# Optimization experiments

Hardware: AMD Instinct MI355X
Metric: run time of the kernel (lower is better)

## Reference

```python
import jax, jax.numpy as jnp
import numpy as np
import math

H, N, B, L = 512, 32, 4, 2048


def setup_inputs() -> dict:
    key = jax.random.key(0)
    ks = jax.random.split(key, 6)
    log_dt_min, log_dt_max = math.log(0.001), math.log(0.01)
    log_dt = jax.random.uniform(ks[0], (H,)) * (log_dt_max - log_dt_min) + log_dt_min
    # A = -0.5 + i*pi*n  =>  log_A_real = log(0.5), A_imag = pi*n
    log_A_real = jnp.full((H, N), math.log(0.5), dtype=jnp.float32)
    A_imag = jnp.broadcast_to(math.pi * jnp.arange(N, dtype=jnp.float32), (H, N))
    # B = ones (complex) stored as real/imag pair
    B_ri = jnp.stack([jnp.ones((N,)), jnp.zeros((N,))], axis=-1).astype(jnp.float32)
    C_ri = jax.random.normal(ks[1], (H, N, 2), dtype=jnp.float32)
    D = jax.random.normal(ks[2], (H,), dtype=jnp.float32)
    W1 = jax.random.normal(ks[3], (H, H), dtype=jnp.float32)
    W2 = jax.random.normal(ks[4], (H, H), dtype=jnp.float32)
    x = jax.random.normal(ks[5], (B, L, H), dtype=jnp.float32)
    return {"input": x, "log_dt": log_dt, "log_A_real": log_A_real,
            "A_imag": A_imag, "B_ri": B_ri, "C_ri": C_ri, "D": D,
            "W1": W1, "W2": W2}


def reference(input, log_dt, log_A_real, A_imag, B_ri, C_ri, D, W1, W2):
    dt = jnp.exp(log_dt)                             # (H,)
    A = -jnp.exp(log_A_real) + 1j * A_imag           # (H,N) complex64
    dtA = (0.5 * dt)[:, None] * A                    # (H,N)
    Ad = (1.0 + dtA) / (1.0 - dtA)                   # bilinear (GBT alpha=0.5) discrete A
    Bc = B_ri[:, 0] + 1j * B_ri[:, 1]                # (N,)
    Bd = dt[:, None] * Bc[None, :] / (1.0 - dtA)     # (H,N) discrete B
    C = C_ri[..., 0] + 1j * C_ri[..., 1]             # (H,N)

    us = jnp.swapaxes(input, 0, 1)                   # (L,B,H)
    x0 = jnp.zeros(input.shape[0:1] + Ad.shape, dtype=Ad.dtype)  # (B,H,N)

    def step(x, u):
        # x: (B,H,N) complex state; u: (B,H) input at one timestep
        x = Ad[None] * x + Bd[None] * u[:, :, None]
        y = jnp.einsum('hn,bhn->bh', C, x).real + D * u
        return x, y

    _, ys = jax.lax.scan(step, x0, us)               # ys: (L,B,H)
    y = jnp.swapaxes(ys, 0, 1)                       # (B,L,H)
    # GLU over stacked projections: (y@W1) * sigmoid(y@W2)
    return (y @ W1) * jax.nn.sigmoid(y @ W2)
```

## Files before the change

### kernel.cpp

```cpp
#include <hip/hip_runtime.h>

#define H_ 512
#define N_ 32
#define B_ 4
#define L_ 2048
#define LC 128
#define NC 16

typedef _Float16 f16x8 __attribute__((ext_vector_type(8)));
typedef float f32x4 __attribute__((ext_vector_type(4)));

__device__ inline unsigned short f2h(float f) {
  _Float16 h = (_Float16)f;
  return __builtin_bit_cast(unsigned short, h);
}
__device__ inline float2 cmul(float2 a, float2 b) {
  return make_float2(fmaf(a.x, b.x, -(a.y * b.y)), fmaf(a.x, b.y, a.y * b.x));
}

#define GLD_LDS16(gsrc, ldst)                                                        \
  __builtin_amdgcn_global_load_lds(                                                  \
      (const __attribute__((address_space(1))) unsigned int*)(gsrc),                 \
      (__attribute__((address_space(3))) unsigned int*)(ldst), 16, 0, 0)

__global__ void transpose_k(const float* __restrict__ in, unsigned short* __restrict__ out) {
  __shared__ float tile[32][33];
  int b = blockIdx.z;
  int t0 = blockIdx.x * 32;
  int h0 = blockIdx.y * 32;
  int tx = threadIdx.x, ty = threadIdx.y;
  const float* src = in + (size_t)b * L_ * H_;
#pragma unroll
  for (int i = 0; i < 32; i += 8)
    tile[ty + i][tx] = src[(size_t)(t0 + ty + i) * H_ + h0 + tx];
  __syncthreads();
  unsigned short* dst = out + (size_t)b * H_ * L_;
#pragma unroll
  for (int i = 0; i < 32; i += 8)
    dst[(size_t)(h0 + ty + i) * L_ + t0 + tx] = f2h(tile[tx][ty + i]);
}

__global__ void wtrans_k(const float* __restrict__ W1, const float* __restrict__ W2,
                         unsigned short* __restrict__ WT1, unsigned short* __restrict__ WT2) {
  __shared__ float tile[32][33];
  const float* W = blockIdx.z ? W2 : W1;
  unsigned short* WT = blockIdx.z ? WT2 : WT1;
  int k0 = blockIdx.x * 32, j0 = blockIdx.y * 32;
  int tx = threadIdx.x, ty = threadIdx.y;
#pragma unroll
  for (int i = 0; i < 32; i += 8)
    tile[ty + i][tx] = W[(size_t)(k0 + ty + i) * H_ + j0 + tx];
  __syncthreads();
#pragma unroll
  for (int i = 0; i < 32; i += 8)
    WT[(size_t)(j0 + ty + i) * H_ + k0 + tx] = f2h(tile[tx][ty + i]);
}

__global__ void ytrans_k(const unsigned short* __restrict__ in, unsigned short* __restrict__ out) {
  __shared__ unsigned short tile[32][34];
  int b = blockIdx.z;
  int t0 = blockIdx.x * 32;
  int h0 = blockIdx.y * 32;
  int tx = threadIdx.x, ty = threadIdx.y;
  const unsigned short* src = in + (size_t)b * H_ * L_;
#pragma unroll
  for (int i = 0; i < 32; i += 8)
    tile[ty + i][tx] = src[(size_t)(h0 + ty + i) * L_ + t0 + tx];
  __syncthreads();
  unsigned short* dst = out + (size_t)b * L_ * H_;
#pragma unroll
  for (int i = 0; i < 32; i += 8)
    dst[(size_t)(t0 + ty + i) * H_ + h0 + tx] = tile[tx][ty + i];
}

#define O_U   0
#define O_BIG 17408
#define O_XEND (O_BIG + 17408)
#define O_XS  52224
#define O_KV  61440
__global__ __launch_bounds__(256) void toeplitz_k(
    const unsigned short* __restrict__ xT,
    const float* __restrict__ log_dt,
    const float* __restrict__ log_A_real,
    const float* __restrict__ A_imag,
    const float* __restrict__ B_ri,
    const float* __restrict__ C_ri,
    const float* __restrict__ Dv,
    unsigned short* __restrict__ yT) {
  __shared__ __align__(16) char slds[61952];
  int h = blockIdx.x;
  int tid = threadIdx.x;
  int wave = tid >> 6, lane = tid & 63;
  int wm = wave >> 1, wn = wave & 1;

  int n = tid & 31, s = tid >> 5;
  float dtv = expf(log_dt[h]);
  float2 Ad, Bd, Cc;
  {
    int idx = (h << 5) + n;
    float ar = -expf(log_A_real[idx]);
    float ai = A_imag[idx];
    float dr = 0.5f * dtv * ar, di = 0.5f * dtv * ai;
    float omr = 1.0f - dr;
    float inv = 1.0f / (omr * omr + di * di);
    Ad = make_float2((1.0f - dr * dr - di * di) * inv, 2.0f * di * inv);
    float br = B_ri[2 * n], bi = B_ri[2 * n + 1];
    Bd = make_float2(dtv * (br * omr - bi * di) * inv, dtv * (br * di + bi * omr) * inv);
    float2 c = ((const float2*)C_ri)[idx];
    Cc = make_float2(c.x, c.y);
  }
  float2 Ad16 = Ad;
#pragma unroll
  for (int q = 0; q < 4; ++q) Ad16 = cmul(Ad16, Ad16);
  float2 AdS = make_float2(1.f, 0.f);
  for (int q = 0; q < s; ++q) AdS = cmul(AdS, Ad16);

  {
    float2 cur = cmul(AdS, Bd);
#pragma unroll
    for (int jj = 0; jj < 16; ++jj) {
      int col = 127 - (s * 16 + jj);
      *(unsigned short*)(slds + O_BIG + n * 272 + col * 2) = f2h(cur.x);
      *(unsigned short*)(slds + O_BIG + (32 + n) * 272 + col * 2) = f2h(cur.y);
      cur = cmul(cur, Ad);
    }
  }
  {
    int bc = tid >> 2, q = tid & 3;
    const uint4* src = (const uint4*)(xT + ((size_t)(bc >> 4) * H_ + h) * L_ + (bc & 15) * 128);
#pragma unroll
    for (int i = 0; i < 4; ++i) {
      uint4 v = src[q * 4 + i];
      *(uint4*)(slds + O_U + bc * 272 + (q * 4 + i) * 16) = v;
    }
  }
  __syncthreads();

  {
    f32x4 acc0[2][2];
#pragma unroll
    for (int mf = 0; mf < 2; ++mf)
#pragma unroll
      for (int nf = 0; nf < 2; ++nf) { f32x4 z; z[0]=z[1]=z[2]=z[3]=0.f; acc0[mf][nf]=z; }
#pragma unroll
    for (int ks = 0; ks < 4; ++ks) {
      int kb = ks * 64 + (lane >> 4) * 16;
      f16x8 a[2], bfr[2];
#pragma unroll
      for (int mf = 0; mf < 2; ++mf)
        a[mf] = *(const f16x8*)(slds + O_BIG + (wm * 32 + mf * 16 + (lane & 15)) * 272 + kb);
#pragma unroll
      for (int nf = 0; nf < 2; ++nf)
        bfr[nf] = *(const f16x8*)(slds + O_U + (wn * 32 + nf * 16 + (lane & 15)) * 272 + kb);
#pragma unroll
      for (int mf = 0; mf < 2; ++mf)
#pragma unroll
        for (int nf = 0; nf < 2; ++nf)
          acc0[mf][nf] = __builtin_amdgcn_mfma_f32_16x16x32_f16(a[mf], bfr[nf], acc0[mf][nf], 0, 0, 0);
    }
    __syncthreads();
#pragma unroll
    for (int mf = 0; mf < 2; ++mf)
#pragma unroll
      for (int nf = 0; nf < 2; ++nf)
#pragma unroll
        for (int r = 0; r < 4; ++r) {
          int row = wm * 32 + mf * 16 + (lane >> 4) * 4 + r;
          int col = wn * 32 + nf * 16 + (lane & 15);
          *(float*)(slds + O_XEND + (row * 68 + col) * 4) = acc0[mf][nf][r];
        }
  }
  __syncthreads();

  if (tid < 128) {
    int nn = tid & 31, b = tid >> 5;
    float2 Ap = Ad;
#pragma unroll
    for (int q = 0; q < 7; ++q) Ap = cmul(Ap, Ap);
    float2 X = make_float2(0.f, 0.f);
    for (int c = 0; c < NC; ++c) {
      int bc = b * 16 + c;
      unsigned int w = (unsigned int)f2h(X.x) | ((unsigned int)f2h(X.y) << 16);
      *(unsigned int*)(slds + O_XS + bc * 144 + nn * 4) = w;
      float er = *(const float*)(slds + O_XEND + (nn * 68 + bc) * 4);
      float ei = *(const float*)(slds + O_XEND + ((32 + nn) * 68 + bc) * 4);
      X = make_float2(fmaf(Ap.x, X.x, fmaf(-Ap.y, X.y, er)),
                      fmaf(Ap.x, X.y, fmaf(Ap.y, X.x, ei)));
    }
  }
  __syncthreads();

  {
    float2 cur = cmul(cmul(Cc, Bd), AdS);
#pragma unroll
    for (int jj = 0; jj < 16; ++jj) {
      int tau = s * 16 + jj;
      *(float*)(slds + O_BIG + (tau * 33 + n) * 4) = cur.x;
      cur = cmul(cur, Ad);
    }
  }
  __syncthreads();
  if (tid < 128) {
    float acc = 0.f;
#pragma unroll
    for (int q = 0; q < 32; ++q)
      acc += *(const float*)(slds + O_BIG + (tid * 33 + q) * 4);
    *(float*)(slds + O_KV + tid * 4) = acc;
  }
  __syncthreads();

  {
    float Dh = Dv[h];
    const float* kv = (const float*)(slds + O_KV);
    int t = tid >> 1, j0 = (tid & 1) * 64;
#pragma unroll
    for (int g = 0; g < 16; ++g) {
      int j = j0 + g * 4;
      unsigned short e[4];
#pragma unroll
      for (int ee = 0; ee < 4; ++ee) {
        int jj = j + ee;
        float v = 0.f;
        if (jj <= t) v = (jj == t) ? (kv[0] + Dh) : kv[t - jj];
        e[ee] = f2h(v);
      }
      unsigned int w0 = (unsigned int)e[0] | ((unsigned int)e[1] << 16);
      unsigned int w1 = (unsigned int)e[2] | ((unsigned int)e[3] << 16);
      *(uint2*)(slds + O_BIG + t * 272 + j * 2) = make_uint2(w0, w1);
    }
  }
  __syncthreads();

  f32x4 accy[4][2];
#pragma unroll
  for (int mf = 0; mf < 4; ++mf)
#pragma unroll
    for (int nf = 0; nf < 2; ++nf) { f32x4 z; z[0]=z[1]=z[2]=z[3]=0.f; accy[mf][nf]=z; }
#pragma unroll
  for (int ks = 0; ks < 4; ++ks) {
    int kb = ks * 64 + (lane >> 4) * 16;
    f16x8 a[4], bfr[2];
#pragma unroll
    for (int mf = 0; mf < 4; ++mf)
      a[mf] = *(const f16x8*)(slds + O_BIG + (wm * 64 + mf * 16 + (lane & 15)) * 272 + kb);
#pragma unroll
    for (int nf = 0; nf < 2; ++nf)
      bfr[nf] = *(const f16x8*)(slds + O_U + (wn * 32 + nf * 16 + (lane & 15)) * 272 + kb);
#pragma unroll
    for (int mf = 0; mf < 4; ++mf)
#pragma unroll
      for (int nf = 0; nf < 2; ++nf)
        accy[mf][nf] = __builtin_amdgcn_mfma_f32_16x16x32_f16(a[mf], bfr[nf], accy[mf][nf], 0, 0, 0);
  }
  __syncthreads();

  {
    float2 cur = cmul(cmul(Cc, Ad), AdS);
#pragma unroll
    for (int jj = 0; jj < 16; ++jj) {
      int t = s * 16 + jj;
      unsigned int w = (unsigned int)f2h(cur.x) | ((unsigned int)f2h(-cur.y) << 16);
      *(unsigned int*)(slds + O_BIG + t * 144 + n * 4) = w;
      cur = cmul(cur, Ad);
    }
  }
  __syncthreads();

#pragma unroll
  for (int ks = 0; ks < 2; ++ks) {
    int kb = ks * 64 + (lane >> 4) * 16;
    f16x8 a[4], bfr[2];
#pragma unroll
    for (int mf = 0; mf < 4; ++mf)
      a[mf] = *(const f16x8*)(slds + O_BIG + (wm * 64 + mf * 16 + (lane & 15)) * 144 + kb);
#pragma unroll
    for (int nf = 0; nf < 2; ++nf)
      bfr[nf] = *(const f16x8*)(slds + O_XS + (wn * 32 + nf * 16 + (lane & 15)) * 144 + kb);
#pragma unroll
    for (int mf = 0; mf < 4; ++mf)
#pragma unroll
      for (int nf = 0; nf < 2; ++nf)
        accy[mf][nf] = __builtin_amdgcn_mfma_f32_16x16x32_f16(a[mf], bfr[nf], accy[mf][nf], 0, 0, 0);
  }
  __syncthreads();

#pragma unroll
  for (int mf = 0; mf < 4; ++mf)
#pragma unroll
    for (int nf = 0; nf < 2; ++nf)
#pragma unroll
      for (int r = 0; r < 4; ++r) {
        int t = wm * 64 + mf * 16 + (lane >> 4) * 4 + r;
        int bc = wn * 32 + nf * 16 + (lane & 15);
        *(float*)(slds + O_BIG + (t * 68 + bc) * 4) = accy[mf][nf][r];
      }
  __syncthreads();
  {
    int bc = tid >> 2, tl = tid & 3;
    unsigned short* dst = yT + ((size_t)(bc >> 4) * H_ + h) * L_ + (bc & 15) * 128;
#pragma unroll
    for (int tt = 0; tt < 16; ++tt) {
      int t = tl * 32 + tt * 2;
      float v0 = *(const float*)(slds + O_BIG + (t * 68 + bc) * 4);
      float v1 = *(const float*)(slds + O_BIG + ((t + 1) * 68 + bc) * 4);
      unsigned int w = (unsigned int)f2h(v0) | ((unsigned int)f2h(v1) << 16);
      *(unsigned int*)(dst + t) = w;
    }
  }
}

__global__ __launch_bounds__(256) void glu_gemm_k(const unsigned short* __restrict__ yN,
                                                  const unsigned short* __restrict__ WT1,
                                                  const unsigned short* __restrict__ WT2,
                                                  float* __restrict__ out) {
  __shared__ __align__(16) char lds[24576];
  int tid = threadIdx.x;
  int m0 = blockIdx.x * 64;
  int n0 = blockIdx.y * 64;
  int wave = tid >> 6, lane = tid & 63;
  int wm = wave >> 1, wn = wave & 1;
  int srow = tid >> 3;
  int scb = (tid & 7) * 16;

  f32x4 acc1[2][2], acc2[2][2];
#pragma unroll
  for (int mf = 0; mf < 2; ++mf)
#pragma unroll
    for (int nf = 0; nf < 2; ++nf) {
      f32x4 z; z[0]=z[1]=z[2]=z[3]=0.f;
      acc1[mf][nf] = z; acc2[mf][nf] = z;
    }

  const char* ybase = (const char*)yN;
  const char* b1base = (const char*)WT1;
  const char* b2base = (const char*)WT2;
  char* As_ = lds;
  char* B1_ = lds + 8192;
  char* B2_ = lds + 16384;

  for (int k0 = 0; k0 < H_; k0 += 64) {
#pragma unroll
    for (int i = 0; i < 2; ++i) {
      int row = i * 32 + srow;
      int sc = scb ^ ((row & 7) << 4);
      GLD_LDS16(ybase + ((size_t)(m0 + row) * H_ + k0) * 2 + sc, As_ + wave * 1024 + i * 4096);
      GLD_LDS16(b1base + ((size_t)(n0 + row) * H_ + k0) * 2 + sc, B1_ + wave * 1024 + i * 4096);
      GLD_LDS16(b2base + ((size_t)(n0 + row) * H_ + k0) * 2 + sc, B2_ + wave * 1024 + i * 4096);
    }
    __syncthreads();
#pragma unroll
    for (int ks = 0; ks < 2; ++ks) {
      f16x8 a[2], b1[2], b2[2];
      int kb = ks * 64 + (lane >> 4) * 16;
#pragma unroll
      for (int mf = 0; mf < 2; ++mf) {
        int row = wm * 32 + mf * 16 + (lane & 15);
        a[mf] = *(const f16x8*)(As_ + row * 128 + (kb ^ ((row & 7) << 4)));
      }
#pragma unroll
      for (int nf = 0; nf < 2; ++nf) {
        int row = wn * 32 + nf * 16 + (lane & 15);
        int off = row * 128 + (kb ^ ((row & 7) << 4));
        b1[nf] = *(const f16x8*)(B1_ + off);
        b2[nf] = *(const f16x8*)(B2_ + off);
      }
#pragma unroll
      for (int mf = 0; mf < 2; ++mf)
#pragma unroll
        for (int nf = 0; nf < 2; ++nf) {
          acc1[mf][nf] = __builtin_amdgcn_mfma_f32_16x16x32_f16(a[mf], b1[nf], acc1[mf][nf], 0, 0, 0);
          acc2[mf][nf] = __builtin_amdgcn_mfma_f32_16x16x32_f16(a[mf], b2[nf], acc2[mf][nf], 0, 0, 0);
        }
    }
    __syncthreads();
  }
  int nb = n0 + wn * 32 + (lane & 15);
  int rbase = (lane >> 4) * 4;
#pragma unroll
  for (int mf = 0; mf < 2; ++mf)
#pragma unroll
    for (int nf = 0; nf < 2; ++nf)
#pragma unroll
      for (int r = 0; r < 4; ++r) {
        int m = m0 + wm * 32 + mf * 16 + rbase + r;
        float g1 = acc1[mf][nf][r];
        float g2 = acc2[mf][nf][r];
        out[(size_t)m * H_ + nb + nf * 16] = g1 / (1.0f + __expf(-g2));
      }
}

extern "C" void kernel_launch(void* const* d_in, const int* in_sizes, int n_in,
                              void* d_out, int out_size, void* d_ws, size_t ws_size,
                              hipStream_t stream) {
  (void)in_sizes; (void)n_in; (void)out_size; (void)ws_size;
  const float* x          = (const float*)d_in[0];
  const float* log_dt     = (const float*)d_in[1];
  const float* log_A_real = (const float*)d_in[2];
  const float* A_imag     = (const float*)d_in[3];
  const float* B_ri       = (const float*)d_in[4];
  const float* C_ri       = (const float*)d_in[5];
  const float* Dv         = (const float*)d_in[6];
  const float* W1         = (const float*)d_in[7];
  const float* W2         = (const float*)d_in[8];
  float* out = (float*)d_out;
  char* ws = (char*)d_ws;

  unsigned short* yN   = (unsigned short*)(ws);
  unsigned short* xT16 = (unsigned short*)(ws + (8u << 20));
  unsigned short* yT   = (unsigned short*)(ws + (16u << 20));
  unsigned short* WT1  = (unsigned short*)(ws + (24u << 20));
  unsigned short* WT2  = (unsigned short*)(ws + (24u << 20) + (512u << 10));

  dim3 tblock(32, 8);
  transpose_k<<<dim3(L_ / 32, H_ / 32, B_), tblock, 0, stream>>>(x, xT16);
  wtrans_k<<<dim3(16, 16, 2), tblock, 0, stream>>>(W1, W2, WT1, WT2);

  toeplitz_k<<<H_, 256, 0, stream>>>(xT16, log_dt, log_A_real, A_imag, B_ri, C_ri, Dv, yT);

  ytrans_k<<<dim3(L_ / 32, H_ / 32, B_), tblock, 0, stream>>>(yT, yN);

  dim3 ggrid((B_ * L_) / 64, H_ / 64);
  glu_gemm_k<<<ggrid, 256, 0, stream>>>(yN, WT1, WT2, out);
}
```

Before: 46.76 us.

## Double toeplitz block to 512 threads, merge transpose kernels, skip zero Toeplitz tiles

Merges the input transpose and the weight transpose into one launch, with extra grid z-slices that return early when unused. The per-channel Toeplitz kernel now runs 512 threads (8 waves), and each wave takes a 16-column MFMA slice instead of 32, so per-thread work is halved. The Ad^s power is now computed by binary exponentiation instead of a serial loop. Waves covering the top row-block do only half of the K steps in the intra-chunk GEMM, skipping zero blocks of the lower-triangular Toeplitz matrix. More waves per block raise parallelism on 512 blocks, at the cost of fewer register-reuse MFMAs per wave and more threads on the barriers.

```diff
diff --git a/kernel.cpp b/kernel.cpp
--- a/kernel.cpp
+++ b/kernel.cpp
@@ -23,12 +23,28 @@
       (const __attribute__((address_space(1))) unsigned int*)(gsrc),                 \
       (__attribute__((address_space(3))) unsigned int*)(ldst), 16, 0, 0)
 
-__global__ void transpose_k(const float* __restrict__ in, unsigned short* __restrict__ out) {
+__global__ void prep_k(const float* __restrict__ in, unsigned short* __restrict__ out,
+                       const float* __restrict__ W1, const float* __restrict__ W2,
+                       unsigned short* __restrict__ WT1, unsigned short* __restrict__ WT2) {
   __shared__ float tile[32][33];
+  int tx = threadIdx.x, ty = threadIdx.y;
+  if (blockIdx.z >= 4) {
+    if (blockIdx.x >= 16) return;
+    const float* W = (blockIdx.z == 5) ? W2 : W1;
+    unsigned short* WT = (blockIdx.z == 5) ? WT2 : WT1;
+    int k0 = blockIdx.x * 32, j0 = blockIdx.y * 32;
+#pragma unroll
+    for (int i = 0; i < 32; i += 8)
+      tile[ty + i][tx] = W[(size_t)(k0 + ty + i) * H_ + j0 + tx];
+    __syncthreads();
+#pragma unroll
+    for (int i = 0; i < 32; i += 8)
+      WT[(size_t)(j0 + ty + i) * H_ + k0 + tx] = f2h(tile[tx][ty + i]);
+    return;
+  }
   int b = blockIdx.z;
   int t0 = blockIdx.x * 32;
   int h0 = blockIdx.y * 32;
-  int tx = threadIdx.x, ty = threadIdx.y;
   const float* src = in + (size_t)b * L_ * H_;
 #pragma unroll
   for (int i = 0; i < 32; i += 8)
@@ -38,22 +54,6 @@
 #pragma unroll
   for (int i = 0; i < 32; i += 8)
     dst[(size_t)(h0 + ty + i) * L_ + t0 + tx] = f2h(tile[tx][ty + i]);
-}
-
-__global__ void wtrans_k(const float* __restrict__ W1, const float* __restrict__ W2,
-                         unsigned short* __restrict__ WT1, unsigned short* __restrict__ WT2) {
-  __shared__ float tile[32][33];
-  const float* W = blockIdx.z ? W2 : W1;
-  unsigned short* WT = blockIdx.z ? WT2 : WT1;
-  int k0 = blockIdx.x * 32, j0 = blockIdx.y * 32;
-  int tx = threadIdx.x, ty = threadIdx.y;
-#pragma unroll
-  for (int i = 0; i < 32; i += 8)
-    tile[ty + i][tx] = W[(size_t)(k0 + ty + i) * H_ + j0 + tx];
-  __syncthreads();
-#pragma unroll
-  for (int i = 0; i < 32; i += 8)
-    WT[(size_t)(j0 + ty + i) * H_ + k0 + tx] = f2h(tile[tx][ty + i]);
 }
 
 __global__ void ytrans_k(const unsigned short* __restrict__ in, unsigned short* __restrict__ out) {
@@ -78,7 +78,7 @@
 #define O_XEND (O_BIG + 17408)
 #define O_XS  52224
 #define O_KV  61440
-__global__ __launch_bounds__(256) void toeplitz_k(
+__global__ __launch_bounds__(512) void toeplitz_k(
     const unsigned short* __restrict__ xT,
     const float* __restrict__ log_dt,
     const float* __restrict__ log_A_real,
@@ -91,9 +91,9 @@
   int h = blockIdx.x;
   int tid = threadIdx.x;
   int wave = tid >> 6, lane = tid & 63;
-  int wm = wave >> 1, wn = wave & 1;
-
-  int n = tid & 31, s = tid >> 5;
+  int wm = wave >> 2, wn = wave & 3;
+
+  int n = tid & 31, s8 = tid >> 5;
   float dtv = expf(log_dt[h]);
   float2 Ad, Bd, Cc;
   {
@@ -109,66 +109,67 @@
     float2 c = ((const float2*)C_ri)[idx];
     Cc = make_float2(c.x, c.y);
   }
-  float2 Ad16 = Ad;
-#pragma unroll
-  for (int q = 0; q < 4; ++q) Ad16 = cmul(Ad16, Ad16);
-  float2 AdS = make_float2(1.f, 0.f);
-  for (int q = 0; q < s; ++q) AdS = cmul(AdS, Ad16);
+  float2 AdS;
+  {
+    float2 p = Ad;
+    p = cmul(p, p); p = cmul(p, p); p = cmul(p, p);
+    float2 acc = make_float2(1.f, 0.f);
+    if (s8 & 1) acc = cmul(acc, p);
+    p = cmul(p, p);
+    if (s8 & 2) acc = cmul(acc, p);
+    p = cmul(p, p);
+    if (s8 & 4) acc = cmul(acc, p);
+    p = cmul(p, p);
+    if (s8 & 8) acc = cmul(acc, p);
+    AdS = acc;
+  }
 
   {
     float2 cur = cmul(AdS, Bd);
 #pragma unroll
-    for (int jj = 0; jj < 16; ++jj) {
-      int col = 127 - (s * 16 + jj);
+    for (int jj = 0; jj < 8; ++jj) {
+      int col = 127 - (s8 * 8 + jj);
       *(unsigned short*)(slds + O_BIG + n * 272 + col * 2) = f2h(cur.x);
       *(unsigned short*)(slds + O_BIG + (32 + n) * 272 + col * 2) = f2h(cur.y);
       cur = cmul(cur, Ad);
     }
   }
   {
-    int bc = tid >> 2, q = tid & 3;
+    int bc = tid >> 3, q = tid & 7;
     const uint4* src = (const uint4*)(xT + ((size_t)(bc >> 4) * H_ + h) * L_ + (bc & 15) * 128);
 #pragma unroll
-    for (int i = 0; i < 4; ++i) {
-      uint4 v = src[q * 4 + i];
-      *(uint4*)(slds + O_U + bc * 272 + (q * 4 + i) * 16) = v;
-    }
-  }
-  __syncthreads();
-
-  {
-    f32x4 acc0[2][2];
-#pragma unroll
-    for (int mf = 0; mf < 2; ++mf)
-#pragma unroll
-      for (int nf = 0; nf < 2; ++nf) { f32x4 z; z[0]=z[1]=z[2]=z[3]=0.f; acc0[mf][nf]=z; }
+    for (int i = 0; i < 2; ++i) {
+      uint4 v = src[q * 2 + i];
+      *(uint4*)(slds + O_U + bc * 272 + (q * 2 + i) * 16) = v;
+    }
+  }
+  __syncthreads();
+
+  {
+    f32x4 acc0[2];
+#pragma unroll
+    for (int mf = 0; mf < 2; ++mf) { f32x4 z; z[0]=z[1]=z[2]=z[3]=0.f; acc0[mf]=z; }
 #pragma unroll
     for (int ks = 0; ks < 4; ++ks) {
       int kb = ks * 64 + (lane >> 4) * 16;
-      f16x8 a[2], bfr[2];
+      f16x8 a[2], bfr;
 #pragma unroll
       for (int mf = 0; mf < 2; ++mf)
         a[mf] = *(const f16x8*)(slds + O_BIG + (wm * 32 + mf * 16 + (lane & 15)) * 272 + kb);
-#pragma unroll
-      for (int nf = 0; nf < 2; ++nf)
-        bfr[nf] = *(const f16x8*)(slds + O_U + (wn * 32 + nf * 16 + (lane & 15)) * 272 + kb);
+      bfr = *(const f16x8*)(slds + O_U + (wn * 16 + (lane & 15)) * 272 + kb);
 #pragma unroll
       for (int mf = 0; mf < 2; ++mf)
-#pragma unroll
-        for (int nf = 0; nf < 2; ++nf)
-          acc0[mf][nf] = __builtin_amdgcn_mfma_f32_16x16x32_f16(a[mf], bfr[nf], acc0[mf][nf], 0, 0, 0);
+        acc0[mf] = __builtin_amdgcn_mfma_f32_16x16x32_f16(a[mf], bfr, acc0[mf], 0, 0, 0);
     }
     __syncthreads();
 #pragma unroll
     for (int mf = 0; mf < 2; ++mf)
 #pragma unroll
-      for (int nf = 0; nf < 2; ++nf)
-#pragma unroll
-        for (int r = 0; r < 4; ++r) {
-          int row = wm * 32 + mf * 16 + (lane >> 4) * 4 + r;
-          int col = wn * 32 + nf * 16 + (lane & 15);
-          *(float*)(slds + O_XEND + (row * 68 + col) * 4) = acc0[mf][nf][r];
-        }
+      for (int r = 0; r < 4; ++r) {
+        int row = wm * 32 + mf * 16 + (lane >> 4) * 4 + r;
+        int col = wn * 16 + (lane & 15);
+        *(float*)(slds + O_XEND + (row * 68 + col) * 4) = acc0[mf][r];
+      }
   }
   __syncthreads();
 
@@ -193,8 +194,8 @@
   {
     float2 cur = cmul(cmul(Cc, Bd), AdS);
 #pragma unroll
-    for (int jj = 0; jj < 16; ++jj) {
-      int tau = s * 16 + jj;
+    for (int jj = 0; jj < 8; ++jj) {
+      int tau = s8 * 8 + jj;
       *(float*)(slds + O_BIG + (tau * 33 + n) * 4) = cur.x;
       cur = cmul(cur, Ad);
     }
@@ -212,9 +213,9 @@
   {
     float Dh = Dv[h];
     const float* kv = (const float*)(slds + O_KV);
-    int t = tid >> 1, j0 = (tid & 1) * 64;
-#pragma unroll
-    for (int g = 0; g < 16; ++g) {
+    int t = tid >> 2, j0 = (tid & 3) * 32;
+#pragma unroll
+    for (int g = 0; g < 8; ++g) {
       int j = j0 + g * 4;
       unsigned short e[4];
 #pragma unroll
@@ -231,34 +232,30 @@
   }
   __syncthreads();
 
-  f32x4 accy[4][2];
-#pragma unroll
-  for (int mf = 0; mf < 4; ++mf)
-#pragma unroll
-    for (int nf = 0; nf < 2; ++nf) { f32x4 z; z[0]=z[1]=z[2]=z[3]=0.f; accy[mf][nf]=z; }
-#pragma unroll
-  for (int ks = 0; ks < 4; ++ks) {
-    int kb = ks * 64 + (lane >> 4) * 16;
-    f16x8 a[4], bfr[2];
-#pragma unroll
-    for (int mf = 0; mf < 4; ++mf)
-      a[mf] = *(const f16x8*)(slds + O_BIG + (wm * 64 + mf * 16 + (lane & 15)) * 272 + kb);
-#pragma unroll
-    for (int nf = 0; nf < 2; ++nf)
-      bfr[nf] = *(const f16x8*)(slds + O_U + (wn * 32 + nf * 16 + (lane & 15)) * 272 + kb);
-#pragma unroll
-    for (int mf = 0; mf < 4; ++mf)
-#pragma unroll
-      for (int nf = 0; nf < 2; ++nf)
-        accy[mf][nf] = __builtin_amdgcn_mfma_f32_16x16x32_f16(a[mf], bfr[nf], accy[mf][nf], 0, 0, 0);
+  f32x4 accy[4];
+#pragma unroll
+  for (int mf = 0; mf < 4; ++mf) { f32x4 z; z[0]=z[1]=z[2]=z[3]=0.f; accy[mf]=z; }
+  {
+    int ksmax = (wm == 0) ? 2 : 4;
+    for (int ks = 0; ks < ksmax; ++ks) {
+      int kb = ks * 64 + (lane >> 4) * 16;
+      f16x8 a[4], bfr;
+#pragma unroll
+      for (int mf = 0; mf < 4; ++mf)
+        a[mf] = *(const f16x8*)(slds + O_BIG + (wm * 64 + mf * 16 + (lane & 15)) * 272 + kb);
+      bfr = *(const f16x8*)(slds + O_U + (wn * 16 + (lane & 15)) * 272 + kb);
+#pragma unroll
+      for (int mf = 0; mf < 4; ++mf)
+        accy[mf] = __builtin_amdgcn_mfma_f32_16x16x32_f16(a[mf], bfr, accy[mf], 0, 0, 0);
+    }
   }
   __syncthreads();
 
   {
     float2 cur = cmul(cmul(Cc, Ad), AdS);
 #pragma unroll
-    for (int jj = 0; jj < 16; ++jj) {
-      int t = s * 16 + jj;
+    for (int jj = 0; jj < 8; ++jj) {
+      int t = s8 * 8 + jj;
       unsigned int w = (unsigned int)f2h(cur.x) | ((unsigned int)f2h(-cur.y) << 16);
       *(unsigned int*)(slds + O_BIG + t * 144 + n * 4) = w;
       cur = cmul(cur, Ad);
@@ -269,38 +266,32 @@
 #pragma unroll
   for (int ks = 0; ks < 2; ++ks) {
     int kb = ks * 64 + (lane >> 4) * 16;
-    f16x8 a[4], bfr[2];
+    f16x8 a[4], bfr;
 #pragma unroll
     for (int mf = 0; mf < 4; ++mf)
       a[mf] = *(const f16x8*)(slds + O_BIG + (wm * 64 + mf * 16 + (lane & 15)) * 144 + kb);
-#pragma unroll
-    for (int nf = 0; nf < 2; ++nf)
-      bfr[nf] = *(const f16x8*)(slds + O_XS + (wn * 32 + nf * 16 + (lane & 15)) * 144 + kb);
+    bfr = *(const f16x8*)(slds + O_XS + (wn * 16 + (lane & 15)) * 144 + kb);
 #pragma unroll
     for (int mf = 0; mf < 4; ++mf)
-#pragma unroll
-      for (int nf = 0; nf < 2; ++nf)
-        accy[mf][nf] = __builtin_amdgcn_mfma_f32_16x16x32_f16(a[mf], bfr[nf], accy[mf][nf], 0, 0, 0);
+      accy[mf] = __builtin_amdgcn_mfma_f32_16x16x32_f16(a[mf], bfr, accy[mf], 0, 0, 0);
   }
   __syncthreads();
 
 #pragma unroll
   for (int mf = 0; mf < 4; ++mf)
 #pragma unroll
-    for (int nf = 0; nf < 2; ++nf)
-#pragma unroll
-      for (int r = 0; r < 4; ++r) {
-        int t = wm * 64 + mf * 16 + (lane >> 4) * 4 + r;
-        int bc = wn * 32 + nf * 16 + (lane & 15);
-        *(float*)(slds + O_BIG + (t * 68 + bc) * 4) = accy[mf][nf][r];
-      }
-  __syncthreads();
-  {
-    int bc = tid >> 2, tl = tid & 3;
+    for (int r = 0; r < 4; ++r) {
+      int t = wm * 64 + mf * 16 + (lane >> 4) * 4 + r;
+      int bc = wn * 16 + (lane & 15);
+      *(float*)(slds + O_BIG + (t * 68 + bc) * 4) = accy[mf][r];
+    }
+  __syncthreads();
+  {
+    int bc = tid >> 3, tl = tid & 7;
     unsigned short* dst = yT + ((size_t)(bc >> 4) * H_ + h) * L_ + (bc & 15) * 128;
 #pragma unroll
-    for (int tt = 0; tt < 16; ++tt) {
-      int t = tl * 32 + tt * 2;
+    for (int tt = 0; tt < 8; ++tt) {
+      int t = tl * 16 + tt * 2;
       float v0 = *(const float*)(slds + O_BIG + (t * 68 + bc) * 4);
       float v1 = *(const float*)(slds + O_BIG + ((t + 1) * 68 + bc) * 4);
       unsigned int w = (unsigned int)f2h(v0) | ((unsigned int)f2h(v1) << 16);
@@ -412,10 +403,9 @@
   unsigned short* WT2  = (unsigned short*)(ws + (24u << 20) + (512u << 10));
 
   dim3 tblock(32, 8);
-  transpose_k<<<dim3(L_ / 32, H_ / 32, B_), tblock, 0, stream>>>(x, xT16);
-  wtrans_k<<<dim3(16, 16, 2), tblock, 0, stream>>>(W1, W2, WT1, WT2);
-
-  toeplitz_k<<<H_, 256, 0, stream>>>(xT16, log_dt, log_A_real, A_imag, B_ri, C_ri, Dv, yT);
+  prep_k<<<dim3(L_ / 32, H_ / 32, 6), tblock, 0, stream>>>(x, xT16, W1, W2, WT1, WT2);
+
+  toeplitz_k<<<H_, 512, 0, stream>>>(xT16, log_dt, log_A_real, A_imag, B_ri, C_ri, Dv, yT);
 
   ytrans_k<<<dim3(L_ / 32, H_ / 32, B_), tblock, 0, stream>>>(yT, yN);
 
```

New measurement: 43.43 us. 7.1% less time.
